# Kernel optimization log

Hardware: AMD Instinct MI355X
Metric: run time of the kernel (lower is better)

## Reference

```python
import jax, jax.numpy as jnp
import numpy as np

B, T, D = 8, 4097, 512
H = 8
WIN = 64


def setup_inputs() -> dict:
    key = jax.random.key(0)
    k1, k2, k3 = jax.random.split(key, 3)
    x = jax.random.normal(k1, (B, T, D), dtype=jnp.float32)
    w_qkv = jax.random.normal(k2, (D, 3 * D), dtype=jnp.float32) * 0.02
    w_out = jax.random.normal(k3, (D, D), dtype=jnp.float32) * 0.02
    return {"x": x, "w_qkv": w_qkv, "w_out": w_out}


def reference(x, w_qkv, w_out):
    b, t, d_model = x.shape
    d = d_model // H
    scale = d ** (-0.5)
    nw = (t - 1) // WIN  # number of full windows over bbox tokens

    qkv = x @ w_qkv  # [B, T, 3D]
    q, k, v = jnp.split(qkv, 3, axis=-1)
    # [B, H, T, d]
    to_heads = lambda z: z.reshape(b, t, H, d).transpose(0, 2, 1, 3)
    q, k, v = to_heads(q), to_heads(k), to_heads(v)

    # global token (index 0) attends to ALL tokens
    q0 = q[:, :, :1]  # [B, H, 1, d]
    attn0 = jax.nn.softmax(jnp.einsum('bhqd,bhkd->bhqk', q0, k) * scale, axis=-1)
    out0 = jnp.einsum('bhqk,bhkd->bhqd', attn0, v)  # [B, H, 1, d]

    # bbox tokens: local attention within non-overlapping windows (no global token in keys)
    qw = q[:, :, 1:].reshape(b, H, nw, WIN, d)
    kw = k[:, :, 1:].reshape(b, H, nw, WIN, d)
    vw = v[:, :, 1:].reshape(b, H, nw, WIN, d)
    s = jnp.einsum('bhnqd,bhnkd->bhnqk', qw, kw) * scale
    attn = jax.nn.softmax(s, axis=-1)
    ow = jnp.einsum('bhnqk,bhnkd->bhnqd', attn, vw).reshape(b, H, t - 1, d)

    out = jnp.concatenate([out0, ow], axis=2)  # [B, H, T, d]
    out = out.transpose(0, 2, 1, 3).reshape(b, t, d_model)
    return out @ w_out
```

## Files before the change

kernel.cpp:

```cpp
#include <hip/hip_runtime.h>
#include <hip/hip_bf16.h>
#include <cstdint>
#include <cstddef>

using bf16 = __hip_bfloat16;
using short8 = __attribute__((ext_vector_type(8))) short;
using f32x4  = __attribute__((ext_vector_type(4))) float;

constexpr int Bc = 8;
constexpr int Tc = 4097;
constexpr int Dc = 512;
constexpr int Hc = 8;
constexpr int Mrows = Bc * Tc;
constexpr int Mpad2 = 33024;
constexpr int NCh = 65;

__device__ __forceinline__ float bf2f(unsigned short u) {
    union { unsigned int i; float f; } v;
    v.i = ((unsigned int)u) << 16;
    return v.f;
}

__device__ __forceinline__ unsigned short f2b(float f) {
    union { float f; unsigned int i; } u; u.f = f;
    unsigned int r = u.i + 0x7FFFu + ((u.i >> 16) & 1u);
    return (unsigned short)(r >> 16);
}

__device__ __forceinline__ void gload_lds16(const void* g, void* l) {
    __builtin_amdgcn_global_load_lds(
        (const __attribute__((address_space(1))) void*)g,
        (__attribute__((address_space(3))) void*)l, 16, 0, 0);
}

template <int N> __device__ __forceinline__ void waitvm() {
    if constexpr (N == 0) asm volatile("s_waitcnt vmcnt(0)" ::: "memory");
    else if constexpr (N == 3) asm volatile("s_waitcnt vmcnt(3)" ::: "memory");
    else if constexpr (N == 4) asm volatile("s_waitcnt vmcnt(4)" ::: "memory");
    else static_assert(N == 0, "unsupported vmcnt");
}

__global__ __launch_bounds__(256)
void k_cvt_x(const float* __restrict__ x, bf16* __restrict__ xb)
{
    size_t i8 = ((size_t)blockIdx.x * 256 + threadIdx.x) * 8;
    if (i8 >= (size_t)Mpad2 * 512) return;
    union { short s[8]; short8 v; } o;
    if (i8 < (size_t)Mrows * 512) {
        float4 v0 = *(const float4*)(x + i8);
        float4 v1 = *(const float4*)(x + i8 + 4);
        o.s[0] = (short)f2b(v0.x); o.s[1] = (short)f2b(v0.y);
        o.s[2] = (short)f2b(v0.z); o.s[3] = (short)f2b(v0.w);
        o.s[4] = (short)f2b(v1.x); o.s[5] = (short)f2b(v1.y);
        o.s[6] = (short)f2b(v1.z); o.s[7] = (short)f2b(v1.w);
    } else {
        o.v = short8{0,0,0,0,0,0,0,0};
    }
    *(short8*)((short*)xb + i8) = o.v;
}

__global__ __launch_bounds__(256)
void k_cvt_wT(const float* __restrict__ w, bf16* __restrict__ wT, int K, int N)
{
    __shared__ float t[32][33];
    int bn = blockIdx.x * 32, bk = blockIdx.y * 32;
    int tx = threadIdx.x & 31, ty = threadIdx.x >> 5;
    #pragma unroll
    for (int j = 0; j < 4; ++j)
        t[ty + j * 8][tx] = w[(size_t)(bk + ty + j * 8) * N + bn + tx];
    __syncthreads();
    #pragma unroll
    for (int j = 0; j < 4; ++j)
        wT[(size_t)(bn + ty + j * 8) * K + bk + tx] =
            __float2bfloat16(t[tx][ty + j * 8]);
}

template <typename OutT, int WR, int WC, int NT, int MINW>
__global__ __launch_bounds__(WR * WC * 64, MINW)
void k_gemm_pipe(const bf16* __restrict__ A, const bf16* __restrict__ Bt,
                 OutT* __restrict__ C, int Mlim)
{
    constexpr int T  = WR * WC * 64;
    constexpr int BM = WR * 64;
    constexpr int BN = WC * 64;
    constexpr int N  = NT * BN;
    constexpr int SZ = (BM + BN) * 32;
    constexpr int LOADS = ((BM + BN) * 4) / T;
    constexpr int NK = 16;
    __shared__ short lds[3 * SZ];

    const int tid  = threadIdx.x;
    const int lane = tid & 63, wave = tid >> 6;
    const int lo = lane & 15, g = lane >> 4;
    const int wr = wave / WC, wc = wave % WC;

    const int nwg = 129 * (BM / 256 == 0 ? 0 : 0) + gridDim.x;
    const int orig = blockIdx.x;
    const int qq = nwg >> 3, rr = nwg & 7;
    const int xc = orig & 7, o8 = orig >> 3;
    const int swz = (xc < rr ? xc * (qq + 1) : rr * (qq + 1) + (xc - rr) * qq) + o8;
    const int bm = (swz / NT) * BM, bn = (swz % NT) * BN;

    const bf16* src[LOADS];
    int dst[LOADS];
    #pragma unroll
    for (int i = 0; i < LOADS; ++i) {
        int d = i * T + tid;
        if (d < BM * 4) {
            int row = d >> 2, c = d & 3, ck = (c - row) & 3;
            src[i] = A + (size_t)(bm + row) * 512 + ck * 8;
            dst[i] = d * 8;
        } else {
            int dd = d - BM * 4;
            int row = dd >> 2, c = dd & 3, ck = (c - row) & 3;
            src[i] = Bt + (size_t)(bn + row) * 512 + ck * 8;
            dst[i] = BM * 32 + dd * 8;
        }
    }

    auto STAGE = [&](int kt, int bb) {
        #pragma unroll
        for (int i = 0; i < LOADS; ++i)
            gload_lds16(src[i] + kt * 32, lds + bb + dst[i]);
    };

    int aoff[4], boff[4];
    #pragma unroll
    for (int i = 0; i < 4; ++i) {
        int ar = wr * 64 + i * 16 + lo;
        aoff[i] = ar * 32 + ((g + ar) & 3) * 8;
        int br = wc * 64 + i * 16 + lo;
        boff[i] = BM * 32 + br * 32 + ((g + br) & 3) * 8;
    }

    f32x4 acc[4][4] = {};

    STAGE(0, 0);
    STAGE(1, SZ);
    waitvm<LOADS>();
    asm volatile("s_barrier" ::: "memory");

    for (int t = 0; t < NK; ++t) {
        const int rb = (t % 3) * SZ;
        if (t < NK - 2) STAGE(t + 2, ((t + 2) % 3) * SZ);

        const short* bufp = lds + rb;
        short8 af[4], bfr[4];
        #pragma unroll
        for (int i = 0; i < 4; ++i) af[i] = *(const short8*)(bufp + aoff[i]);
        #pragma unroll
        for (int i = 0; i < 4; ++i) bfr[i] = *(const short8*)(bufp + boff[i]);

        __builtin_amdgcn_s_setprio(1);
        #pragma unroll
        for (int mi = 0; mi < 4; ++mi)
            #pragma unroll
            for (int ni = 0; ni < 4; ++ni)
                acc[mi][ni] = __builtin_amdgcn_mfma_f32_16x16x32_bf16(
                    bfr[ni], af[mi], acc[mi][ni], 0, 0, 0);
        __builtin_amdgcn_s_setprio(0);

        asm volatile("s_waitcnt lgkmcnt(0)" ::: "memory");
        if (t < NK - 2)       waitvm<LOADS>();
        else if (t == NK - 2) waitvm<0>();
        if (t < NK - 1) asm volatile("s_barrier" ::: "memory");
    }

    #pragma unroll
    for (int mi = 0; mi < 4; ++mi) {
        int m = bm + wr * 64 + mi * 16 + lo;
        if (m < Mlim) {
            #pragma unroll
            for (int ni = 0; ni < 4; ++ni) {
                int n = bn + wc * 64 + ni * 16 + g * 4;
                if constexpr (sizeof(OutT) == 2) {
                    ushort4 o = { f2b(acc[mi][ni][0]), f2b(acc[mi][ni][1]),
                                  f2b(acc[mi][ni][2]), f2b(acc[mi][ni][3]) };
                    *(ushort4*)((bf16*)C + (size_t)m * N + n) = o;
                } else {
                    float4 o = { acc[mi][ni][0], acc[mi][ni][1],
                                 acc[mi][ni][2], acc[mi][ni][3] };
                    *(float4*)((float*)C + (size_t)m * N + n) = o;
                }
            }
        }
    }
}

__global__ __launch_bounds__(256)
void k_attn_win(const bf16* __restrict__ qkv, bf16* __restrict__ aout)
{
    __shared__ __attribute__((aligned(16))) unsigned short pS[64 * 64];
    __shared__ __attribute__((aligned(16))) unsigned short vT[64 * 64];

    const int n = blockIdx.x, h = blockIdx.y, b = blockIdx.z;
    const int tid = threadIdx.x;
    const int wave = tid >> 6, lane = tid & 63;
    const int lo = lane & 15, g = lane >> 4;

    const bf16* base = qkv + ((size_t)b * Tc + 1 + (size_t)n * 64) * 1536 + h * 64;
    const bf16* kbase = base + 512;
    const bf16* vbase = base + 1024;

    {
        const int key = tid & 63;
        const int d0 = (tid >> 6) * 16;
        const bf16* vp = vbase + (size_t)key * 1536 + d0;
        ushort4 u[4];
        #pragma unroll
        for (int q = 0; q < 4; ++q) u[q] = *(const ushort4*)(vp + q * 4);
        const unsigned short vals[16] = {
            u[0].x, u[0].y, u[0].z, u[0].w, u[1].x, u[1].y, u[1].z, u[1].w,
            u[2].x, u[2].y, u[2].z, u[2].w, u[3].x, u[3].y, u[3].z, u[3].w };
        #pragma unroll
        for (int j = 0; j < 16; ++j) {
            int d = d0 + j;
            int byteoff = d * 128 + ((key * 2) ^ ((d & 7) << 4));
            *(unsigned short*)((char*)vT + byteoff) = vals[j];
        }
    }

    short8 qf[2];
    {
        const bf16* qp = base + (size_t)(wave * 16 + lo) * 1536 + g * 8;
        qf[0] = *(const short8*)(qp);
        qf[1] = *(const short8*)(qp + 32);
    }

    f32x4 sacc[4] = {};
    #pragma unroll
    for (int ni = 0; ni < 4; ++ni) {
        const bf16* kp = kbase + (size_t)(ni * 16 + lo) * 1536 + g * 8;
        short8 k0 = *(const short8*)(kp);
        short8 k1 = *(const short8*)(kp + 32);
        sacc[ni] = __builtin_amdgcn_mfma_f32_16x16x32_bf16(qf[0], k0, sacc[ni], 0, 0, 0);
        sacc[ni] = __builtin_amdgcn_mfma_f32_16x16x32_bf16(qf[1], k1, sacc[ni], 0, 0, 0);
    }

    __syncthreads();

    float pv[4][4];
    float inv[4];
    #pragma unroll
    for (int r = 0; r < 4; ++r) {
        float m = fmaxf(fmaxf(sacc[0][r], sacc[1][r]),
                        fmaxf(sacc[2][r], sacc[3][r])) * 0.125f;
        m = fmaxf(m, __shfl_xor(m, 1));
        m = fmaxf(m, __shfl_xor(m, 2));
        m = fmaxf(m, __shfl_xor(m, 4));
        m = fmaxf(m, __shfl_xor(m, 8));
        float s = 0.f;
        #pragma unroll
        for (int ni = 0; ni < 4; ++ni) {
            float e = __expf(sacc[ni][r] * 0.125f - m);
            pv[ni][r] = e;
            s += e;
        }
        s += __shfl_xor(s, 1);
        s += __shfl_xor(s, 2);
        s += __shfl_xor(s, 4);
        s += __shfl_xor(s, 8);
        inv[r] = 1.f / s;
    }

    #pragma unroll
    for (int ni = 0; ni < 4; ++ni) {
        #pragma unroll
        for (int r = 0; r < 4; ++r) {
            int qrow = wave * 16 + g * 4 + r;
            int col = ni * 16 + lo;
            int byteoff = qrow * 128 + ((col * 2) ^ ((qrow & 7) << 4));
            *(unsigned short*)((char*)pS + byteoff) = f2b(pv[ni][r]);
        }
    }
    __syncthreads();

    f32x4 oacc[4] = {};
    #pragma unroll
    for (int s = 0; s < 2; ++s) {
        int arow2 = wave * 16 + lo;
        int abyte = arow2 * 128 + (((s * 32 + g * 8) * 2) ^ ((arow2 & 7) << 4));
        short8 pa = *(const short8*)((const char*)pS + abyte);
        #pragma unroll
        for (int nd = 0; nd < 4; ++nd) {
            int d = nd * 16 + lo;
            int bbyte = d * 128 + (((s * 32 + g * 8) * 2) ^ ((d & 7) << 4));
            short8 vb = *(const short8*)((const char*)vT + bbyte);
            oacc[nd] = __builtin_amdgcn_mfma_f32_16x16x32_bf16(pa, vb, oacc[nd], 0, 0, 0);
        }
    }

    #pragma unroll
    for (int nd = 0; nd < 4; ++nd) {
        #pragma unroll
        for (int r = 0; r < 4; ++r) {
            int t = 1 + n * 64 + wave * 16 + g * 4 + r;
            aout[((size_t)b * Tc + t) * Dc + h * 64 + nd * 16 + lo] =
                __float2bfloat16(oacc[nd][r] * inv[r]);
        }
    }
}

__global__ __launch_bounds__(64)
void k_tok0_part(const bf16* __restrict__ qkv, float* __restrict__ part)
{
    const int c = blockIdx.x, h = blockIdx.y, b = blockIdx.z;
    const int lane = threadIdx.x;
    __shared__ float q0s[64];
    __shared__ float vS[64][65];
    __shared__ float pSm[64];

    q0s[lane] = bf2f(*(const unsigned short*)
        (qkv + (size_t)b * Tc * 1536 + h * 64 + lane));
    __syncthreads();

    const int t = c * 64 + lane;
    const bool valid = t < Tc;
    float logit = -1e30f;
    if (valid) {
        const bf16* kp = qkv + ((size_t)b * Tc + t) * 1536 + 512 + h * 64;
        float l = 0.f;
        #pragma unroll
        for (int d4 = 0; d4 < 16; ++d4) {
            ushort4 ku = ((const ushort4*)kp)[d4];
            l = fmaf(q0s[d4 * 4 + 0], bf2f(ku.x), l);
            l = fmaf(q0s[d4 * 4 + 1], bf2f(ku.y), l);
            l = fmaf(q0s[d4 * 4 + 2], bf2f(ku.z), l);
            l = fmaf(q0s[d4 * 4 + 3], bf2f(ku.w), l);
        }
        logit = l * 0.125f;
        const bf16* vp = kp + 512;
        #pragma unroll
        for (int d4 = 0; d4 < 16; ++d4) {
            ushort4 vu = ((const ushort4*)vp)[d4];
            vS[lane][d4 * 4 + 0] = bf2f(vu.x);
            vS[lane][d4 * 4 + 1] = bf2f(vu.y);
            vS[lane][d4 * 4 + 2] = bf2f(vu.z);
            vS[lane][d4 * 4 + 3] = bf2f(vu.w);
        }
    } else {
        #pragma unroll
        for (int d = 0; d < 64; ++d) vS[lane][d] = 0.f;
    }

    float m = logit;
    #pragma unroll
    for (int off = 1; off < 64; off <<= 1) m = fmaxf(m, __shfl_xor(m, off));
    float p = valid ? __expf(logit - m) : 0.f;
    float s = p;
    #pragma unroll
    for (int off = 1; off < 64; off <<= 1) s += __shfl_xor(s, off);
    pSm[lane] = p;
    __syncthreads();

    float o = 0.f;
    #pragma unroll
    for (int i = 0; i < 64; ++i) o = fmaf(pSm[i], vS[i][lane], o);

    float* pout = part + ((size_t)(b * Hc + h) * NCh + c) * 66;
    pout[lane] = o;
    if (lane == 0) { pout[64] = m; pout[65] = s; }
}

__global__ __launch_bounds__(64)
void k_tok0_reduce(const float* __restrict__ part, bf16* __restrict__ aout)
{
    const int h = blockIdx.x, b = blockIdx.y;
    const int lane = threadIdx.x;
    const float* base = part + (size_t)(b * Hc + h) * NCh * 66;

    float M = -1e30f;
    for (int c = 0; c < NCh; ++c) M = fmaxf(M, base[c * 66 + 64]);

    float S = 0.f, o = 0.f;
    for (int c = 0; c < NCh; ++c) {
        const float* pp = base + c * 66;
        float w = __expf(pp[64] - M);
        S += pp[65] * w;
        o = fmaf(pp[lane], w, o);
    }
    aout[(size_t)b * Tc * Dc + h * 64 + lane] = __float2bfloat16(o / S);
}

extern "C" void kernel_launch(void* const* d_in, const int* in_sizes, int n_in,
                              void* d_out, int out_size, void* d_ws, size_t ws_size,
                              hipStream_t stream)
{
    const float* x     = (const float*)d_in[0];
    const float* w_qkv = (const float*)d_in[1];
    const float* w_out = (const float*)d_in[2];
    float* out = (float*)d_out;

    bf16* qkv = (bf16*)d_ws;
    bf16* xa  = qkv + (size_t)Mrows * 1536;
    bf16* wqT = xa  + (size_t)Mpad2 * 512;
    bf16* woT = wqT + (size_t)1536 * 512;
    float* part = (float*)wqT;

    {
        int nblk = (int)(((size_t)Mpad2 * 512 / 8 + 255) / 256);
        k_cvt_x<<<nblk, 256, 0, stream>>>(x, xa);
    }
    k_cvt_wT<<<dim3(48, 16), 256, 0, stream>>>(w_qkv, wqT, 512, 1536);
    k_cvt_wT<<<dim3(16, 16), 256, 0, stream>>>(w_out, woT, 512, 512);

    k_gemm_pipe<bf16, 4, 2, 12, 4><<<129 * 12, 512, 0, stream>>>(
        xa, wqT, qkv, Mrows);

    k_attn_win<<<dim3(64, Hc, Bc), 256, 0, stream>>>(qkv, xa);
    k_tok0_part<<<dim3(NCh, Hc, Bc), dim3(64), 0, stream>>>(qkv, part);
    k_tok0_reduce<<<dim3(Hc, Bc), dim3(64), 0, stream>>>(part, xa);

    k_gemm_pipe<float, 2, 2, 4, 3><<<257 * 4, 256, 0, stream>>>(
        xa, woT, out, Mrows);
}
```

Baseline: 196.5 us.

## Use fixed 128x128 GEMM tiles with 4-stage LDS pipeline and new swizzle

Replaces the templated GEMM with a fixed 128x128-tile, 256-thread kernel that prefetches three k-steps ahead through a 4-buffer LDS ring instead of two ahead through 3 buffers. The LDS chunk swizzle now rotates on row pairs rather than single rows, to change the bank-conflict pattern of the fragment reads. The QKV GEMM moves from 256x128 tiles with 512 threads to 128x128 tiles with twice as many workgroups. The aim is to hide more global-load latency, at the cost of more LDS per block (64 KB), which may limit occupancy.

```diff
diff --git a/kernel.cpp b/kernel.cpp
--- a/kernel.cpp
+++ b/kernel.cpp
@@ -35,8 +35,8 @@
 
 template <int N> __device__ __forceinline__ void waitvm() {
     if constexpr (N == 0) asm volatile("s_waitcnt vmcnt(0)" ::: "memory");
-    else if constexpr (N == 3) asm volatile("s_waitcnt vmcnt(3)" ::: "memory");
     else if constexpr (N == 4) asm volatile("s_waitcnt vmcnt(4)" ::: "memory");
+    else if constexpr (N == 8) asm volatile("s_waitcnt vmcnt(8)" ::: "memory");
     else static_assert(N == 0, "unsupported vmcnt");
 }
 
@@ -75,26 +75,24 @@
             __float2bfloat16(t[tx][ty + j * 8]);
 }
 
-template <typename OutT, int WR, int WC, int NT, int MINW>
-__global__ __launch_bounds__(WR * WC * 64, MINW)
-void k_gemm_pipe(const bf16* __restrict__ A, const bf16* __restrict__ Bt,
-                 OutT* __restrict__ C, int Mlim)
-{
-    constexpr int T  = WR * WC * 64;
-    constexpr int BM = WR * 64;
-    constexpr int BN = WC * 64;
-    constexpr int N  = NT * BN;
+template <typename OutT, int NT>
+__global__ __launch_bounds__(256, 2)
+void k_gemm_q4(const bf16* __restrict__ A, const bf16* __restrict__ Bt,
+               OutT* __restrict__ C, int Mlim)
+{
+    constexpr int BM = 128, BN = 128;
+    constexpr int N  = NT * 128;
     constexpr int SZ = (BM + BN) * 32;
-    constexpr int LOADS = ((BM + BN) * 4) / T;
+    constexpr int LOADS = 4;
     constexpr int NK = 16;
-    __shared__ short lds[3 * SZ];
+    __shared__ short lds[4 * SZ];
 
     const int tid  = threadIdx.x;
     const int lane = tid & 63, wave = tid >> 6;
     const int lo = lane & 15, g = lane >> 4;
-    const int wr = wave / WC, wc = wave % WC;
-
-    const int nwg = 129 * (BM / 256 == 0 ? 0 : 0) + gridDim.x;
+    const int wr = wave >> 1, wc = wave & 1;
+
+    const int nwg = gridDim.x;
     const int orig = blockIdx.x;
     const int qq = nwg >> 3, rr = nwg & 7;
     const int xc = orig & 7, o8 = orig >> 3;
@@ -105,20 +103,21 @@
     int dst[LOADS];
     #pragma unroll
     for (int i = 0; i < LOADS; ++i) {
-        int d = i * T + tid;
+        int d = i * 256 + tid;
         if (d < BM * 4) {
-            int row = d >> 2, c = d & 3, ck = (c - row) & 3;
+            int row = d >> 2, c = d & 3, ck = (c - (row >> 1)) & 3;
             src[i] = A + (size_t)(bm + row) * 512 + ck * 8;
             dst[i] = d * 8;
         } else {
             int dd = d - BM * 4;
-            int row = dd >> 2, c = dd & 3, ck = (c - row) & 3;
+            int row = dd >> 2, c = dd & 3, ck = (c - (row >> 1)) & 3;
             src[i] = Bt + (size_t)(bn + row) * 512 + ck * 8;
             dst[i] = BM * 32 + dd * 8;
         }
     }
 
-    auto STAGE = [&](int kt, int bb) {
+    auto STAGE = [&](int kt) {
+        const int bb = (kt & 3) * SZ;
         #pragma unroll
         for (int i = 0; i < LOADS; ++i)
             gload_lds16(src[i] + kt * 32, lds + bb + dst[i]);
@@ -128,23 +127,21 @@
     #pragma unroll
     for (int i = 0; i < 4; ++i) {
         int ar = wr * 64 + i * 16 + lo;
-        aoff[i] = ar * 32 + ((g + ar) & 3) * 8;
+        aoff[i] = ar * 32 + ((g + (ar >> 1)) & 3) * 8;
         int br = wc * 64 + i * 16 + lo;
-        boff[i] = BM * 32 + br * 32 + ((g + br) & 3) * 8;
+        boff[i] = BM * 32 + br * 32 + ((g + (br >> 1)) & 3) * 8;
     }
 
     f32x4 acc[4][4] = {};
 
-    STAGE(0, 0);
-    STAGE(1, SZ);
-    waitvm<LOADS>();
+    STAGE(0); STAGE(1); STAGE(2);
+    waitvm<8>();
     asm volatile("s_barrier" ::: "memory");
 
     for (int t = 0; t < NK; ++t) {
-        const int rb = (t % 3) * SZ;
-        if (t < NK - 2) STAGE(t + 2, ((t + 2) % 3) * SZ);
-
-        const short* bufp = lds + rb;
+        if (t < NK - 3) STAGE(t + 3);
+
+        const short* bufp = lds + (t & 3) * SZ;
         short8 af[4], bfr[4];
         #pragma unroll
         for (int i = 0; i < 4; ++i) af[i] = *(const short8*)(bufp + aoff[i]);
@@ -161,7 +158,8 @@
         __builtin_amdgcn_s_setprio(0);
 
         asm volatile("s_waitcnt lgkmcnt(0)" ::: "memory");
-        if (t < NK - 2)       waitvm<LOADS>();
+        if (t < NK - 3)       waitvm<8>();
+        else if (t == NK - 3) waitvm<4>();
         else if (t == NK - 2) waitvm<0>();
         if (t < NK - 1) asm volatile("s_barrier" ::: "memory");
     }
@@ -404,13 +402,11 @@
     k_cvt_wT<<<dim3(48, 16), 256, 0, stream>>>(w_qkv, wqT, 512, 1536);
     k_cvt_wT<<<dim3(16, 16), 256, 0, stream>>>(w_out, woT, 512, 512);
 
-    k_gemm_pipe<bf16, 4, 2, 12, 4><<<129 * 12, 512, 0, stream>>>(
-        xa, wqT, qkv, Mrows);
+    k_gemm_q4<bf16, 12><<<257 * 12, 256, 0, stream>>>(xa, wqT, qkv, Mrows);
 
     k_attn_win<<<dim3(64, Hc, Bc), 256, 0, stream>>>(qkv, xa);
     k_tok0_part<<<dim3(NCh, Hc, Bc), dim3(64), 0, stream>>>(qkv, part);
     k_tok0_reduce<<<dim3(Hc, Bc), dim3(64), 0, stream>>>(part, xa);
 
-    k_gemm_pipe<float, 2, 2, 4, 3><<<257 * 4, 256, 0, stream>>>(
-        xa, woT, out, Mrows);
-}
+    k_gemm_q4<float, 4><<<257 * 4, 256, 0, stream>>>(xa, woT, out, Mrows);
+}
```

After: 201.4 us. 1.03x slower.
